# Kernel optimization log

Measured on AMD Instinct MI355X. Metric: run time of the kernel, lower is better.

## Reference

```python
import jax, jax.numpy as jnp
import numpy as np

NEG_SLOPE = 0.2


def gat_conv(x, edge_index, W, att_src, att_dst, bias, concat):
    # PyG GATConv with add_self_loops=True, negative_slope=0.2
    N = x.shape[0]
    H, C = att_src.shape
    h = (x @ W).reshape(N, H, C)                      # [N, H, C]
    loops = jnp.arange(N, dtype=edge_index.dtype)
    src = jnp.concatenate([edge_index[0], loops])     # [E+N]
    dst = jnp.concatenate([edge_index[1], loops])
    a_src = jnp.einsum('nhc,hc->nh', h, att_src)      # [N, H]
    a_dst = jnp.einsum('nhc,hc->nh', h, att_dst)
    e = jax.nn.leaky_relu(a_src[src] + a_dst[dst], NEG_SLOPE)  # [E+N, H]
    # segment softmax over destination neighborhoods
    e_max = jax.ops.segment_max(e, dst, num_segments=N)        # [N, H]
    e_exp = jnp.exp(e - e_max[dst])
    denom = jax.ops.segment_sum(e_exp, dst, num_segments=N)    # [N, H]
    alpha = e_exp / denom[dst]                                  # [E+N, H]
    msg = h[src] * alpha[:, :, None]                            # [E+N, H, C]
    out = jax.ops.segment_sum(msg, dst, num_segments=N)        # [N, H, C]
    if concat:
        out = out.reshape(N, H * C)
    else:
        out = out.mean(axis=1)
    return out + bias


def setup_inputs() -> dict:
    key = jax.random.key(0)
    ks = jax.random.split(key, 12)
    N, E = 100000, 1600000
    IN, HID, HEADS = 8, 32, 4
    x = jax.random.normal(ks[0], (N, IN), dtype=jnp.float32)
    edge_index = jax.random.randint(ks[1], (2, E), 0, N, dtype=jnp.int32)
    s = 0.1
    W1 = jax.random.normal(ks[2], (IN, HEADS * HID), dtype=jnp.float32) * s
    att_src1 = jax.random.normal(ks[3], (HEADS, HID), dtype=jnp.float32) * s
    att_dst1 = jax.random.normal(ks[4], (HEADS, HID), dtype=jnp.float32) * s
    bias1 = jnp.zeros((HEADS * HID,), dtype=jnp.float32)
    W2 = jax.random.normal(ks[5], (HEADS * HID, HEADS * HID), dtype=jnp.float32) * s
    att_src2 = jax.random.normal(ks[6], (HEADS, HID), dtype=jnp.float32) * s
    att_dst2 = jax.random.normal(ks[7], (HEADS, HID), dtype=jnp.float32) * s
    bias2 = jnp.zeros((HID,), dtype=jnp.float32)
    W_lin = jax.random.normal(ks[8], (HID, 1), dtype=jnp.float32) * s
    b_lin = jnp.zeros((1,), dtype=jnp.float32)
    return {"x": x, "edge_index": edge_index,
            "W1": W1, "att_src1": att_src1, "att_dst1": att_dst1, "bias1": bias1,
            "W2": W2, "att_src2": att_src2, "att_dst2": att_dst2, "bias2": bias2,
            "W_lin": W_lin, "b_lin": b_lin}


def reference(x, edge_index, W1, att_src1, att_dst1, bias1,
              W2, att_src2, att_dst2, bias2, W_lin, b_lin):
    h = gat_conv(x, edge_index, W1, att_src1, att_dst1, bias1, concat=True)
    h = jax.nn.relu(h)
    # dropout p=0.2 is a no-op in eval mode
    h = gat_conv(h, edge_index, W2, att_src2, att_dst2, bias2, concat=False)
    h = jax.nn.relu(h)
    out = h @ W_lin + b_lin
    return out.reshape(-1)
```

## Files before the change

kernel.cpp:

```cpp
#include <hip/hip_runtime.h>

#define NEG_SLOPE 0.2f
#define K1 1024
#define S1B 512

typedef __attribute__((ext_vector_type(8))) short bf16x8;
typedef __attribute__((ext_vector_type(4))) float f32x4;

__device__ __forceinline__ unsigned short f2b(float f) {
    unsigned int u = __float_as_uint(f);
    u += 0x7FFFu + ((u >> 16) & 1u);
    return (unsigned short)(u >> 16);
}
__device__ __forceinline__ float blo(unsigned int u) { return __uint_as_float(u << 16); }
__device__ __forceinline__ float bhi(unsigned int u) { return __uint_as_float(u & 0xFFFF0000u); }

__device__ __forceinline__ void tofs_scan(const int* __restrict__ T,
                                          int* sT, int* ps, int t)
{
    int base = t * 4;
    int s0 = T[base], s1 = T[base + 1], s2 = T[base + 2], s3 = T[base + 3];
    int tot = s0 + s1 + s2 + s3;
    ps[t] = tot;
    __syncthreads();
    for (int off = 1; off < 256; off <<= 1) {
        int u = (t >= off) ? ps[t - off] : 0;
        __syncthreads();
        ps[t] += u;
        __syncthreads();
    }
    int excl = ps[t] - tot;
    sT[base]     = excl;
    sT[base + 1] = excl + s0;
    sT[base + 2] = excl + s0 + s1;
    sT[base + 3] = excl + s0 + s1 + s2;
    __syncthreads();
}

__global__ __launch_bounds__(256) void k_lsort(
    const int* __restrict__ ei, int E, int EN,
    int2* __restrict__ pairs,
    unsigned int* __restrict__ tmp,
    const float* __restrict__ x, const float* __restrict__ W1,
    const float* __restrict__ as1, const float* __restrict__ ad1,
    float* __restrict__ asrc, float* __restrict__ adst,
    const float* __restrict__ W2, unsigned short* __restrict__ W2p,
    int N, int AB)
{
    int b = blockIdx.x;
    int t = threadIdx.x;
    if (b < S1B) {
        __shared__ int hist[K1];
        __shared__ int ofs[K1];
        __shared__ int cur[K1];
        __shared__ int ps[256];
        for (int k = t; k < K1; k += 256) hist[k] = 0;
        __syncthreads();
        int chunk = (EN + S1B - 1) / S1B;
        int lo = b * chunk, hi = min(lo + chunk, EN);
        for (int e = lo + t; e < hi; e += 256) {
            int dst = (e < E) ? ei[E + e] : (e - E);
            atomicAdd(&hist[dst >> 7], 1);
        }
        __syncthreads();
        int base = t * 4;
        int h0 = hist[base], h1 = hist[base + 1];
        int h2 = hist[base + 2], h3 = hist[base + 3];
        int tot = h0 + h1 + h2 + h3;
        ps[t] = tot;
        __syncthreads();
        for (int off = 1; off < 256; off <<= 1) {
            int u = (t >= off) ? ps[t - off] : 0;
            __syncthreads();
            ps[t] += u;
            __syncthreads();
        }
        int ex = ps[t] - tot;
        ofs[base]     = ex;
        ofs[base + 1] = ex + h0;
        ofs[base + 2] = ex + h0 + h1;
        ofs[base + 3] = ex + h0 + h1 + h2;
        __syncthreads();
        for (int k = t; k < K1; k += 256) {
            pairs[(size_t)b * K1 + k] = make_int2(ofs[k], hist[k]);
            cur[k] = ofs[k];
        }
        __syncthreads();
        for (int e = lo + t; e < hi; e += 256) {
            int src, dst;
            if (e < E) { src = ei[e]; dst = ei[E + e]; }
            else       { src = dst = e - E; }
            int pos = lo + atomicAdd(&cur[dst >> 7], 1);
            tmp[pos] = ((unsigned int)src << 7) | (unsigned int)(dst & 127);
        }
        return;
    }
    if (b < S1B + AB) {
        __shared__ float s_wa[32], s_wd[32];
        if (t < 32) {
            int k = t >> 2, hh = t & 3;
            float sa = 0.f, sd = 0.f;
            for (int cc = 0; cc < 32; cc++) {
                float w = W1[k * 128 + hh * 32 + cc];
                sa = fmaf(w, as1[hh * 32 + cc], sa);
                sd = fmaf(w, ad1[hh * 32 + cc], sd);
            }
            s_wa[t] = sa;
            s_wd[t] = sd;
        }
        __syncthreads();
        int g = (b - S1B) * 256 + t;
        int n = g >> 2;
        if (n >= N) return;
        int hh = g & 3;
        const float* xr = x + (size_t)n * 8;
        float sa = 0.f, sd = 0.f;
        #pragma unroll
        for (int k = 0; k < 8; k++) {
            float xv = xr[k];
            sa = fmaf(xv, s_wa[k * 4 + hh], sa);
            sd = fmaf(xv, s_wd[k * 4 + hh], sd);
        }
        asrc[n * 4 + hh] = sa;
        adst[n * 4 + hh] = sd;
        return;
    }
    int w = t >> 6, lane = t & 63;
    int quad = lane >> 4, lanelo = lane & 15;
    int tile_n = b - S1B - AB;
    size_t base = (((size_t)tile_n * 4 + w) * 64 + lane) * 8;
    #pragma unroll
    for (int j = 0; j < 8; j++) {
        int k = w * 32 + quad * 8 + j;
        int n = tile_n * 16 + lanelo;
        W2p[base + j] = f2b(W2[k * 128 + n]);
    }
}

__global__ __launch_bounds__(256) void k_colsum(
    const int2* __restrict__ pairs, int* __restrict__ T)
{
    __shared__ int part[256];
    int j = blockIdx.x, t = threadIdx.x;
    int kk = t & 15;
    int bs = t >> 4;
    int k = j * 16 + kk;
    int s = 0;
    for (int b = bs; b < S1B; b += 16)
        s += pairs[(size_t)b * K1 + k].y;
    part[t] = s;
    __syncthreads();
    for (int off = 128; off >= 16; off >>= 1) {
        if (t < off) part[t] += part[t + off];
        __syncthreads();
    }
    if (t < 16) T[j * 16 + t] = part[t];
}

__global__ __launch_bounds__(256) void k_fine2(
    const int2* __restrict__ pairs, const unsigned int* __restrict__ tmp,
    const int* __restrict__ T,
    int* __restrict__ esrc, int* __restrict__ rowptr, int N, int EN)
{
    __shared__ int sT[K1];
    __shared__ int ps[256];
    __shared__ int rofs[S1B], rcnt[S1B], sofs[S1B];
    __shared__ unsigned int stg[3072];
    __shared__ int hist[128], scn[128];
    int k = blockIdx.x, t = threadIdx.x;
    tofs_scan(T, sT, ps, t);
    int lo = sT[k];
    int nbase = k << 7;
    if (k == K1 - 1 && t == 0) rowptr[N] = EN;
    if (nbase >= N) return;
    int chunk = (EN + S1B - 1) / S1B;

    #pragma unroll
    for (int i = 0; i < 2; i++) {
        int b = t + i * 256;
        int2 pr = pairs[(size_t)b * K1 + k];
        rofs[b] = pr.x;
        rcnt[b] = pr.y;
    }
    __syncthreads();
    int c0 = rcnt[2 * t], c1 = rcnt[2 * t + 1];
    int tot = c0 + c1;
    ps[t] = tot;
    __syncthreads();
    for (int off = 1; off < 256; off <<= 1) {
        int u = (t >= off) ? ps[t - off] : 0;
        __syncthreads();
        ps[t] += u;
        __syncthreads();
    }
    int ex = ps[t] - tot;
    sofs[2 * t] = ex;
    sofs[2 * t + 1] = ex + c0;
    __syncthreads();
    int total = sofs[S1B - 1] + rcnt[S1B - 1];
    #pragma unroll
    for (int i = 0; i < 2; i++) {
        int b = t + i * 256;
        int n0 = rcnt[b], o = sofs[b];
        const unsigned int* srcp = tmp + (size_t)b * chunk + rofs[b];
        for (int q = 0; q < n0; q++) stg[o + q] = srcp[q];
    }
    if (t < 128) hist[t] = 0;
    __syncthreads();
    for (int i = t; i < total; i += 256)
        atomicAdd(&hist[stg[i] & 127], 1);
    __syncthreads();
    int v = (t < 128) ? hist[t] : 0;
    if (t < 128) scn[t] = v;
    __syncthreads();
    for (int off = 1; off < 128; off <<= 1) {
        int u = (t >= off && t < 128) ? scn[t - off] : 0;
        __syncthreads();
        if (t < 128) scn[t] += u;
        __syncthreads();
    }
    if (t < 128) {
        int o = scn[t] - v;
        int dst = nbase + t;
        if (dst < N) rowptr[dst] = lo + o;
        hist[t] = o;
    }
    __syncthreads();
    for (int i = t; i < total; i += 256) {
        unsigned int e = stg[i];
        int r = atomicAdd(&hist[e & 127], 1);
        esrc[lo + r] = (int)(e >> 7);
    }
}

__global__ __launch_bounds__(256) void k_l1f2(
    const int* __restrict__ rowptr, const int* __restrict__ esrc,
    const float* __restrict__ x,
    const float* __restrict__ asrc1, const float* __restrict__ adst1,
    const float* __restrict__ W1, const float* __restrict__ bias1,
    const unsigned short* __restrict__ W2p,
    const float* __restrict__ att_src, const float* __restrict__ att_dst,
    unsigned short* __restrict__ h, float* __restrict__ asrc2,
    float* __restrict__ adst2, int N)
{
    __shared__ float s_y[32][36];
    __shared__ float s_d[32][4];
    __shared__ uint4 s_tile[512];
    char* s_a = reinterpret_cast<char*>(s_tile);
    int t = threadIdx.x;
    int mbase = blockIdx.x * 32;

    {
        int nl = t >> 3;
        int node = mbase + nl;
        if (node >= N) node = N - 1;
        int l8 = t & 7;
        int eo = l8 & 3;
        int dh = (l8 >> 2) << 2;
        const float4* a4p = reinterpret_cast<const float4*>(asrc1);
        float4 ad4 = *reinterpret_cast<const float4*>(adst1 + (size_t)node * 4);
        float acc[4][4];
        #pragma unroll
        for (int hh = 0; hh < 4; hh++)
            #pragma unroll
            for (int c = 0; c < 4; c++) acc[hh][c] = 0.f;
        float d4[4] = {0.f, 0.f, 0.f, 0.f};
        int start = rowptr[node], end = rowptr[node + 1];
        int jj = start + eo;
        for (; jj + 4 < end; jj += 8) {
            int s0 = esrc[jj], s1 = esrc[jj + 4];
            float4 a0 = a4p[s0], a1 = a4p[s1];
            float4 x0 = *reinterpret_cast<const float4*>(x + (size_t)s0 * 8 + dh);
            float4 x1 = *reinterpret_cast<const float4*>(x + (size_t)s1 * 8 + dh);
            float w0[4], w1[4];
            float a;
            a = a0.x + ad4.x; a = a > 0.f ? a : NEG_SLOPE * a; w0[0] = __expf(a);
            a = a0.y + ad4.y; a = a > 0.f ? a : NEG_SLOPE * a; w0[1] = __expf(a);
            a = a0.z + ad4.z; a = a > 0.f ? a : NEG_SLOPE * a; w0[2] = __expf(a);
            a = a0.w + ad4.w; a = a > 0.f ? a : NEG_SLOPE * a; w0[3] = __expf(a);
            a = a1.x + ad4.x; a = a > 0.f ? a : NEG_SLOPE * a; w1[0] = __expf(a);
            a = a1.y + ad4.y; a = a > 0.f ? a : NEG_SLOPE * a; w1[1] = __expf(a);
            a = a1.z + ad4.z; a = a > 0.f ? a : NEG_SLOPE * a; w1[2] = __expf(a);
            a = a1.w + ad4.w; a = a > 0.f ? a : NEG_SLOPE * a; w1[3] = __expf(a);
            #pragma unroll
            for (int hh = 0; hh < 4; hh++) {
                acc[hh][0] = fmaf(w0[hh], x0.x, acc[hh][0]);
                acc[hh][1] = fmaf(w0[hh], x0.y, acc[hh][1]);
                acc[hh][2] = fmaf(w0[hh], x0.z, acc[hh][2]);
                acc[hh][3] = fmaf(w0[hh], x0.w, acc[hh][3]);
                acc[hh][0] = fmaf(w1[hh], x1.x, acc[hh][0]);
                acc[hh][1] = fmaf(w1[hh], x1.y, acc[hh][1]);
                acc[hh][2] = fmaf(w1[hh], x1.z, acc[hh][2]);
                acc[hh][3] = fmaf(w1[hh], x1.w, acc[hh][3]);
                d4[hh] += w0[hh] + w1[hh];
            }
        }
        if (jj < end) {
            int s0 = esrc[jj];
            float4 a0 = a4p[s0];
            float4 x0 = *reinterpret_cast<const float4*>(x + (size_t)s0 * 8 + dh);
            float w0[4];
            float a;
            a = a0.x + ad4.x; a = a > 0.f ? a : NEG_SLOPE * a; w0[0] = __expf(a);
            a = a0.y + ad4.y; a = a > 0.f ? a : NEG_SLOPE * a; w0[1] = __expf(a);
            a = a0.z + ad4.z; a = a > 0.f ? a : NEG_SLOPE * a; w0[2] = __expf(a);
            a = a0.w + ad4.w; a = a > 0.f ? a : NEG_SLOPE * a; w0[3] = __expf(a);
            #pragma unroll
            for (int hh = 0; hh < 4; hh++) {
                acc[hh][0] = fmaf(w0[hh], x0.x, acc[hh][0]);
                acc[hh][1] = fmaf(w0[hh], x0.y, acc[hh][1]);
                acc[hh][2] = fmaf(w0[hh], x0.z, acc[hh][2]);
                acc[hh][3] = fmaf(w0[hh], x0.w, acc[hh][3]);
                d4[hh] += w0[hh];
            }
        }
        #pragma unroll
        for (int hh = 0; hh < 4; hh++) {
            #pragma unroll
            for (int c = 0; c < 4; c++) {
                acc[hh][c] += __shfl_xor(acc[hh][c], 1, 64);
                acc[hh][c] += __shfl_xor(acc[hh][c], 2, 64);
            }
            d4[hh] += __shfl_xor(d4[hh], 1, 64);
            d4[hh] += __shfl_xor(d4[hh], 2, 64);
        }
        if (eo == 0) {
            #pragma unroll
            for (int hh = 0; hh < 4; hh++) {
                float4 o = {acc[hh][0], acc[hh][1], acc[hh][2], acc[hh][3]};
                *reinterpret_cast<float4*>(&s_y[nl][hh * 8 + dh]) = o;
            }
            if (dh == 0) {
                float4 od = {d4[0], d4[1], d4[2], d4[3]};
                *reinterpret_cast<float4*>(&s_d[nl][0]) = od;
            }
        }
    }
    __syncthreads();

    {
        int nl = t >> 3;
        int seg = t & 7;
        int head = seg >> 1;
        float inv = 1.f / s_d[nl][head];
        float y8[8];
        #pragma unroll
        for (int k = 0; k < 8; k++) y8[k] = s_y[nl][head * 8 + k];
        int c0 = seg * 16;
        float acc16[16];
        #pragma unroll
        for (int c = 0; c < 16; c++) acc16[c] = 0.f;
        #pragma unroll
        for (int k = 0; k < 8; k++) {
            float yk = y8[k];
            const float4* wr = reinterpret_cast<const float4*>(W1 + k * 128 + c0);
            #pragma unroll
            for (int q = 0; q < 4; q++) {
                float4 wv = wr[q];
                acc16[q * 4 + 0] = fmaf(yk, wv.x, acc16[q * 4 + 0]);
                acc16[q * 4 + 1] = fmaf(yk, wv.y, acc16[q * 4 + 1]);
                acc16[q * 4 + 2] = fmaf(yk, wv.z, acc16[q * 4 + 2]);
                acc16[q * 4 + 3] = fmaf(yk, wv.w, acc16[q * 4 + 3]);
            }
        }
        unsigned int dw[8];
        #pragma unroll
        for (int c = 0; c < 8; c++) {
            float v0 = acc16[2 * c]     * inv + bias1[c0 + 2 * c];
            float v1 = acc16[2 * c + 1] * inv + bias1[c0 + 2 * c + 1];
            v0 = v0 > 0.f ? v0 : 0.f;
            v1 = v1 > 0.f ? v1 : 0.f;
            dw[c] = ((unsigned int)f2b(v1) << 16) | f2b(v0);
        }
        int byte0 = nl * 256 + seg * 32;
        int swz = (nl & 7) << 4;
        *reinterpret_cast<uint4*>(&s_a[byte0 ^ swz]) =
            make_uint4(dw[0], dw[1], dw[2], dw[3]);
        *reinterpret_cast<uint4*>(&s_a[(byte0 + 16) ^ swz]) =
            make_uint4(dw[4], dw[5], dw[6], dw[7]);
    }
    __syncthreads();

    int w = t >> 6;
    int lane = t & 63;
    int quad = lane >> 4, lanelo = lane & 15;
    int wcb = w * 32;

    f32x4 acc[2][2];
    #pragma unroll
    for (int rt = 0; rt < 2; rt++)
        #pragma unroll
        for (int ct = 0; ct < 2; ct++)
            acc[rt][ct] = (f32x4){0.f, 0.f, 0.f, 0.f};

    #pragma unroll
    for (int kc = 0; kc < 4; kc++) {
        bf16x8 a[2], b[2];
        #pragma unroll
        for (int rt = 0; rt < 2; rt++) {
            int nl = rt * 16 + lanelo;
            int byte = nl * 256 + kc * 64 + quad * 16;
            a[rt] = *reinterpret_cast<const bf16x8*>(&s_a[byte ^ ((nl & 7) << 4)]);
        }
        #pragma unroll
        for (int ct = 0; ct < 2; ct++) {
            int tile_n = w * 2 + ct;
            b[ct] = *reinterpret_cast<const bf16x8*>(
                W2p + (((size_t)tile_n * 4 + kc) * 64 + lane) * 8);
        }
        #pragma unroll
        for (int rt = 0; rt < 2; rt++)
            #pragma unroll
            for (int ct = 0; ct < 2; ct++)
                acc[rt][ct] = __builtin_amdgcn_mfma_f32_16x16x32_bf16(
                    a[rt], b[ct], acc[rt][ct], 0, 0, 0);
    }

    float as_[2], ad_[2];
    #pragma unroll
    for (int ct = 0; ct < 2; ct++) {
        int col = wcb + ct * 16 + lanelo;
        as_[ct] = att_src[col];
        ad_[ct] = att_dst[col];
    }
    #pragma unroll
    for (int rt = 0; rt < 2; rt++) {
        #pragma unroll
        for (int reg = 0; reg < 4; reg++) {
            int node = mbase + rt * 16 + quad * 4 + reg;
            bool ok = node < N;
            float v0 = acc[rt][0][reg], v1 = acc[rt][1][reg];
            if (ok) {
                h[(size_t)node * 128 + wcb + lanelo]      = f2b(v0);
                h[(size_t)node * 128 + wcb + 16 + lanelo] = f2b(v1);
            }
            float ps = v0 * as_[0] + v1 * as_[1];
            float pd = v0 * ad_[0] + v1 * ad_[1];
            #pragma unroll
            for (int off = 8; off >= 1; off >>= 1) {
                ps += __shfl_xor(ps, off, 64);
                pd += __shfl_xor(pd, off, 64);
            }
            if (ok && lanelo == 0) {
                asrc2[node * 4 + w] = ps;
                adst2[node * 4 + w] = pd;
            }
        }
    }
}

__device__ __forceinline__ void agg_edge(float w, uint4 u, float acc[8])
{
    acc[0] = fmaf(w, blo(u.x), acc[0]); acc[1] = fmaf(w, bhi(u.x), acc[1]);
    acc[2] = fmaf(w, blo(u.y), acc[2]); acc[3] = fmaf(w, bhi(u.y), acc[3]);
    acc[4] = fmaf(w, blo(u.z), acc[4]); acc[5] = fmaf(w, bhi(u.z), acc[5]);
    acc[6] = fmaf(w, blo(u.w), acc[6]); acc[7] = fmaf(w, bhi(u.w), acc[7]);
}

__device__ __forceinline__ void agg_core16(
    int n, int l4,
    const int* __restrict__ rowptr, const int* __restrict__ esrc,
    const uint4* __restrict__ h ,
    const float* __restrict__ asrc, const float* __restrict__ adst,
    float acc[8], float& d)
{
    int head = l4 >> 2;
    float ad = adst[n * 4 + head];
    #pragma unroll
    for (int k = 0; k < 8; k++) acc[k] = 0.f;
    d = 0.f;
    int j = rowptr[n], end = rowptr[n + 1];

    for (; j + 4 <= end; j += 4) {
        int s0 = esrc[j], s1 = esrc[j + 1], s2 = esrc[j + 2], s3 = esrc[j + 3];
        float A0 = asrc[s0 * 4 + head];
        float A1 = asrc[s1 * 4 + head];
        float A2 = asrc[s2 * 4 + head];
        float A3 = asrc[s3 * 4 + head];
        uint4 u0 = h[(size_t)s0 * 16 + l4];
        uint4 u1 = h[(size_t)s1 * 16 + l4];
        uint4 u2 = h[(size_t)s2 * 16 + l4];
        uint4 u3 = h[(size_t)s3 * 16 + l4];
        A0 += ad; A0 = A0 > 0.f ? A0 : NEG_SLOPE * A0; float w0 = __expf(A0);
        A1 += ad; A1 = A1 > 0.f ? A1 : NEG_SLOPE * A1; float w1 = __expf(A1);
        A2 += ad; A2 = A2 > 0.f ? A2 : NEG_SLOPE * A2; float w2 = __expf(A2);
        A3 += ad; A3 = A3 > 0.f ? A3 : NEG_SLOPE * A3; float w3 = __expf(A3);
        agg_edge(w0, u0, acc); d += w0;
        agg_edge(w1, u1, acc); d += w1;
        agg_edge(w2, u2, acc); d += w2;
        agg_edge(w3, u3, acc); d += w3;
    }
    for (; j < end; j++) {
        int src = esrc[j];
        float a = asrc[src * 4 + head] + ad;
        a = a > 0.f ? a : NEG_SLOPE * a;
        float w = __expf(a);
        uint4 u = h[(size_t)src * 16 + l4];
        agg_edge(w, u, acc); d += w;
    }
}

__global__ __launch_bounds__(256) void k_agg2(
    const int* __restrict__ rowptr, const int* __restrict__ esrc,
    const uint4* __restrict__ h, const float* __restrict__ asrc,
    const float* __restrict__ adst, const float* __restrict__ bias2,
    const float* __restrict__ Wlin, const float* __restrict__ blin,
    float* __restrict__ out, int N)
{
    int gid = blockIdx.x * 256 + threadIdx.x;
    int node = gid >> 4;
    if (node >= N) return;
    int l4 = threadIdx.x & 15;
    float acc[8], d;
    agg_core16(node, l4, rowptr, esrc, h, asrc, adst, acc, d);
    float inv = 1.f / d;
    float v[8];
    #pragma unroll
    for (int k = 0; k < 8; k++) v[k] = acc[k] * inv;
    #pragma unroll
    for (int k = 0; k < 8; k++) {
        v[k] += __shfl_xor(v[k], 4, 64);
        v[k] += __shfl_xor(v[k], 8, 64);
    }
    int cc = (l4 & 3) * 8;
    const float4 b0 = *reinterpret_cast<const float4*>(bias2 + cc);
    const float4 b1 = *reinterpret_cast<const float4*>(bias2 + cc + 4);
    const float4 w0 = *reinterpret_cast<const float4*>(Wlin + cc);
    const float4 w1 = *reinterpret_cast<const float4*>(Wlin + cc + 4);
    float bb[8] = {b0.x, b0.y, b0.z, b0.w, b1.x, b1.y, b1.z, b1.w};
    float ww[8] = {w0.x, w0.y, w0.z, w0.w, w1.x, w1.y, w1.z, w1.w};
    float t = 0.f;
    #pragma unroll
    for (int k = 0; k < 8; k++) {
        float m = 0.25f * v[k] + bb[k];
        float y = m > 0.f ? m : 0.f;
        t = fmaf(y, ww[k], t);
    }
    t += __shfl_xor(t, 1, 64);
    t += __shfl_xor(t, 2, 64);
    if (l4 == 0) out[node] = t + blin[0];
}

extern "C" void kernel_launch(void* const* d_in, const int* in_sizes, int n_in,
                              void* d_out, int out_size, void* d_ws, size_t ws_size,
                              hipStream_t stream)
{
    const float* x   = (const float*)d_in[0];
    const int*   ei  = (const int*)  d_in[1];
    const float* W1  = (const float*)d_in[2];
    const float* as1 = (const float*)d_in[3];
    const float* ad1 = (const float*)d_in[4];
    const float* b1  = (const float*)d_in[5];
    const float* W2  = (const float*)d_in[6];
    const float* as2 = (const float*)d_in[7];
    const float* ad2 = (const float*)d_in[8];
    const float* b2  = (const float*)d_in[9];
    const float* Wl  = (const float*)d_in[10];
    const float* bl  = (const float*)d_in[11];
    float* out = (float*)d_out;

    int N  = in_sizes[0] / 8;
    int E  = in_sizes[1] / 2;
    int EN = E + N;

    float* ws    = (float*)d_ws;
    unsigned short* A = (unsigned short*)ws;
    float* asrc1 = ws + (size_t)N * 64;
    float* adst1 = asrc1 + (size_t)N * 4;
    float* asrc2 = adst1 + (size_t)N * 4;
    float* adst2 = asrc2 + (size_t)N * 4;
    int* rowptr  = (int*)(adst2 + (size_t)N * 4);
    int* esrc    = rowptr + (N + 1);
    int* T       = esrc + EN;
    unsigned short* W2p = (unsigned short*)(T + K1);
    uintptr_t pp = (uintptr_t)(W2p + 16384);
    pp = (pp + 7) & ~(uintptr_t)7;
    int2* pairs  = (int2*)pp;
    unsigned int* tmp = (unsigned int*)(pairs + (size_t)S1B * K1);

    int ab = (N + 63) / 64;
    int nb = (N + 15) / 16;

    k_lsort<<<S1B + ab + 8, 256, 0, stream>>>(ei, E, EN, pairs, tmp,
                                              x, W1, as1, ad1, asrc1, adst1,
                                              W2, W2p, N, ab);
    k_colsum<<<K1 / 16, 256, 0, stream>>>(pairs, T);
    k_fine2<<<K1, 256, 0, stream>>>(pairs, tmp, T, esrc, rowptr, N, EN);

    k_l1f2<<<(N + 31) / 32, 256, 0, stream>>>(rowptr, esrc, x, asrc1, adst1,
                                              W1, b1, W2p, as2, ad2,
                                              A, asrc2, adst2, N);
    k_agg2<<<nb, 256, 0, stream>>>(rowptr, esrc, (const uint4*)A,
                                   asrc2, adst2, b2, Wl, bl, out, N);
}
```

Measured before the change: 255.9 us.

## Parallelize attention-weight precompute and bucket copy, split layer-1 launch in halves

```diff
diff --git a/kernel.cpp b/kernel.cpp
--- a/kernel.cpp
+++ b/kernel.cpp
@@ -97,16 +97,23 @@
     }
     if (b < S1B + AB) {
         __shared__ float s_wa[32], s_wd[32];
-        if (t < 32) {
-            int k = t >> 2, hh = t & 3;
-            float sa = 0.f, sd = 0.f;
-            for (int cc = 0; cc < 32; cc++) {
-                float w = W1[k * 128 + hh * 32 + cc];
-                sa = fmaf(w, as1[hh * 32 + cc], sa);
-                sd = fmaf(w, ad1[hh * 32 + cc], sd);
-            }
-            s_wa[t] = sa;
-            s_wd[t] = sd;
+        {
+            int oid = t >> 2, part = t & 3;
+            int k = (oid & 31) >> 2, hh = oid & 3;
+            const float* av = (oid < 32) ? as1 : ad1;
+            float s = 0.f;
+            int cc0 = part * 8;
+            #pragma unroll
+            for (int i = 0; i < 8; i++) {
+                float w = W1[k * 128 + hh * 32 + cc0 + i];
+                s = fmaf(w, av[hh * 32 + cc0 + i], s);
+            }
+            s += __shfl_xor(s, 1, 64);
+            s += __shfl_xor(s, 2, 64);
+            if (part == 0) {
+                if (oid < 32) s_wa[oid] = s;
+                else          s_wd[oid - 32] = s;
+            }
         }
         __syncthreads();
         int g = (b - S1B) * 256 + t;
@@ -199,11 +206,13 @@
     __syncthreads();
     int total = sofs[S1B - 1] + rcnt[S1B - 1];
     #pragma unroll
-    for (int i = 0; i < 2; i++) {
-        int b = t + i * 256;
+    for (int p = 0; p < 8; p++) {
+        int b = p * 64 + (t >> 2);
+        int lj = t & 3;
         int n0 = rcnt[b], o = sofs[b];
         const unsigned int* srcp = tmp + (size_t)b * chunk + rofs[b];
-        for (int q = 0; q < n0; q++) stg[o + q] = srcp[q];
+        for (int q = lj; q < n0; q += 4)
+            stg[o + q] = srcp[q];
     }
     if (t < 128) hist[t] = 0;
     __syncthreads();
@@ -241,14 +250,14 @@
     const unsigned short* __restrict__ W2p,
     const float* __restrict__ att_src, const float* __restrict__ att_dst,
     unsigned short* __restrict__ h, float* __restrict__ asrc2,
-    float* __restrict__ adst2, int N)
+    float* __restrict__ adst2, int N, int n0)
 {
     __shared__ float s_y[32][36];
     __shared__ float s_d[32][4];
     __shared__ uint4 s_tile[512];
     char* s_a = reinterpret_cast<char*>(s_tile);
     int t = threadIdx.x;
-    int mbase = blockIdx.x * 32;
+    int mbase = n0 + blockIdx.x * 32;
 
     {
         int nl = t >> 3;
@@ -580,6 +589,9 @@
 
     int ab = (N + 63) / 64;
     int nb = (N + 15) / 16;
+    int half = ((N / 2) + 31) & ~31;
+    int nba = half / 32;
+    int nbb = (N - half + 31) / 32;
 
     k_lsort<<<S1B + ab + 8, 256, 0, stream>>>(ei, E, EN, pairs, tmp,
                                               x, W1, as1, ad1, asrc1, adst1,
@@ -587,9 +599,12 @@
     k_colsum<<<K1 / 16, 256, 0, stream>>>(pairs, T);
     k_fine2<<<K1, 256, 0, stream>>>(pairs, tmp, T, esrc, rowptr, N, EN);
 
-    k_l1f2<<<(N + 31) / 32, 256, 0, stream>>>(rowptr, esrc, x, asrc1, adst1,
-                                              W1, b1, W2p, as2, ad2,
-                                              A, asrc2, adst2, N);
+    k_l1f2<<<nba, 256, 0, stream>>>(rowptr, esrc, x, asrc1, adst1,
+                                    W1, b1, W2p, as2, ad2,
+                                    A, asrc2, adst2, N, 0);
+    k_l1f2<<<nbb, 256, 0, stream>>>(rowptr, esrc, x, asrc1, adst1,
+                                    W1, b1, W2p, as2, ad2,
+                                    A, asrc2, adst2, N, half);
     k_agg2<<<nb, 256, 0, stream>>>(rowptr, esrc, (const uint4*)A,
                                    asrc2, adst2, b2, Wl, bl, out, N);
 }
```

New measurement: 263.6 us. 1.03x slower.
